# Optimization experiments

Hardware: AMD Instinct MI355X
Metric: run time of the kernel (lower is better)

The kernel has to match this reference:

```python
import jax, jax.numpy as jnp
import numpy as np

MU = 0.9
STEP = 0.1
BETA = 0.999
EPS = 1e-6

N, H, D, M = 256, 16, 64, 64


def elu_feature_map(x):
    # elu(x) + 1, applied to last dim of queries/keys
    return jax.nn.elu(x) + 1.0


def setup_inputs() -> dict:
    key = jax.random.key(0)
    ks = jax.random.split(key, 7)
    return {
        "query": jax.random.normal(ks[0], (N, H, D), dtype=jnp.float32),
        "key": jax.random.normal(ks[1], (N, H, D), dtype=jnp.float32),
        "value": jax.random.normal(ks[2], (N, H, M), dtype=jnp.float32),
        "Si": jax.random.normal(ks[3], (N, H, D, M), dtype=jnp.float32) * 0.1,
        "Zi": jax.random.uniform(ks[4], (N, H, D), dtype=jnp.float32),
        "Pi": jax.random.normal(ks[5], (N, H, D, M), dtype=jnp.float32) * 0.1,
        "Mi": jax.random.uniform(ks[6], (N, H, D, M), dtype=jnp.float32),
        "time_indx": 5,
    }


def reference(query, key, value, Si, Zi, Pi, Mi, time_indx):
    t = time_indx + 1  # Python int -> branch below is static
    Q = elu_feature_map(query)  # (N,H,D)
    K = elu_feature_map(key)    # (N,H,D)

    Zi = Zi + K
    Ui = jnp.einsum('nhd,nhm->nhdm', K, value)  # outer product per (n,h)
    Pi = (MU * Pi - STEP * Ui) * ((1.0 - MU) / (STEP * (1.0 - MU ** t)))
    Mi = BETA * Mi + (1.0 - BETA) * (Ui * Ui)

    rho = 2.0 / (1.0 - BETA) - 1.0
    rhoi = rho - 2.0 * t * BETA ** t / (1.0 - BETA ** t)
    if rhoi > 4.0:
        ri = float(np.sqrt((rhoi - 4.0) * (rhoi - 2.0) * rho
                           / ((rho - 4.0) * (rho - 2.0) * rhoi)))
        Si = Si - Pi * ri / jnp.sqrt(Mi / (1.0 - BETA ** t) + 1e-16)
    else:
        Si = Si - Pi

    Z = 1.0 / (jnp.einsum('nhd,nhd->nh', Q, Zi) + EPS)       # (N,H)
    V = jnp.einsum('nhd,nhdm,nh->nhm', Q, Si, Z)              # (N,H,M)
    return (V, Si, Zi, Pi, Mi)
```

## Files before the change

### kernel.cpp

```cpp
#include <hip/hip_runtime.h>
#include <cmath>

#define D 64
#define M 64

typedef float f4 __attribute__((ext_vector_type(4)));

__global__ __launch_bounds__(256) void raa_kernel(
    const float* __restrict__ q, const float* __restrict__ kk,
    const float* __restrict__ vv, const float* __restrict__ Si,
    const float* __restrict__ Zi, const float* __restrict__ Pi,
    const float* __restrict__ Mi, const int* __restrict__ tind,
    float* __restrict__ oV, float* __restrict__ oSi, float* __restrict__ oZi,
    float* __restrict__ oPi, float* __restrict__ oMi)
{
  const int nh = blockIdx.x;
  const int t  = threadIdx.x;
  const int base = nh * D;
  const int big  = nh * (D * M);

  __shared__ float sQ[D];
  __shared__ float sK[D];
  __shared__ float sVv[M];
  __shared__ float sZ1;
  __shared__ float vred[4][16][4];

  const int ti = tind[0] + 1;
  const double td = (double)ti;
  const double mu_t   = pow(0.9, td);
  const double beta_t = pow(0.999, td);
  const float c1     = (float)(1.0 / (1.0 - mu_t));
  const float inv_bc = (float)(1.0 / (1.0 - beta_t));
  const double rho  = 2.0 / (1.0 - 0.999) - 1.0;
  const double rhoi = rho - 2.0 * td * beta_t / (1.0 - beta_t);
  const bool  use_ri = (rhoi > 4.0);
  const float ri = use_ri
      ? (float)sqrt((rhoi - 4.0) * (rhoi - 2.0) * rho /
                    ((rho - 4.0) * (rho - 2.0) * rhoi))
      : 0.0f;
  const float muf   = 0.9f;
  const float stepf = 0.1f;
  const float betaf = 0.999f;
  const float ombf  = (float)(1.0 - 0.999);

  const int tx = t & 15;
  const int ty = t >> 4;
  const int off0 = big + ty * M + tx * 4;
  f4 pi[4], mi[4], si[4];
#pragma unroll
  for (int j = 0; j < 4; ++j) {
    const int off = off0 + j * (16 * M);
    pi[j] = __builtin_nontemporal_load((const f4*)&Pi[off]);
    mi[j] = __builtin_nontemporal_load((const f4*)&Mi[off]);
    si[j] = __builtin_nontemporal_load((const f4*)&Si[off]);
  }

  if (t < D) {
    const float x = q[base + t];
    const float y = kk[base + t];
    const float Qv = x > 0.f ? x + 1.f : expf(x);
    const float Kv = y > 0.f ? y + 1.f : expf(y);
    const float zn = Zi[base + t] + Kv;
    sQ[t] = Qv;
    sK[t] = Kv;
    sVv[t] = vv[base + t];
    oZi[base + t] = zn;
    float p = Qv * zn;
    p += __shfl_xor(p, 1);
    p += __shfl_xor(p, 2);
    p += __shfl_xor(p, 4);
    p += __shfl_xor(p, 8);
    p += __shfl_xor(p, 16);
    p += __shfl_xor(p, 32);
    if (t == 0) sZ1 = 1.0f / (p + 1e-6f);
  }
  __syncthreads();

  const f4 val4 = *(const f4*)&sVv[tx * 4];
  f4 acc = (f4)(0.f);

#pragma unroll
  for (int j = 0; j < 4; ++j) {
    const int d = ty + 16 * j;
    const int off = off0 + j * (16 * M);
    const float Kd = sK[d];
    const float Qd = sQ[d];

    f4 u  = Kd * val4;
    f4 pn = (muf * pi[j] - stepf * u) * c1;
    f4 mn = betaf * mi[j] + ombf * (u * u);
    __builtin_nontemporal_store(pn, (f4*)&oPi[off]);
    __builtin_nontemporal_store(mn, (f4*)&oMi[off]);

    f4 sn;
    if (use_ri) {
      sn.x = si[j].x - pn.x * ri * rsqrtf(mn.x * inv_bc + 1e-16f);
      sn.y = si[j].y - pn.y * ri * rsqrtf(mn.y * inv_bc + 1e-16f);
      sn.z = si[j].z - pn.z * ri * rsqrtf(mn.z * inv_bc + 1e-16f);
      sn.w = si[j].w - pn.w * ri * rsqrtf(mn.w * inv_bc + 1e-16f);
    } else {
      sn = si[j] - pn;
    }
    __builtin_nontemporal_store(sn, (f4*)&oSi[off]);

    acc += Qd * sn;
  }

  acc.x += __shfl_xor(acc.x, 16); acc.x += __shfl_xor(acc.x, 32);
  acc.y += __shfl_xor(acc.y, 16); acc.y += __shfl_xor(acc.y, 32);
  acc.z += __shfl_xor(acc.z, 16); acc.z += __shfl_xor(acc.z, 32);
  acc.w += __shfl_xor(acc.w, 16); acc.w += __shfl_xor(acc.w, 32);

  const int wave = t >> 6;
  const int lane = t & 63;
  if (lane < 16) {
    vred[wave][lane][0] = acc.x;
    vred[wave][lane][1] = acc.y;
    vred[wave][lane][2] = acc.z;
    vred[wave][lane][3] = acc.w;
  }
  __syncthreads();

  if (t < M) {
    const int mtx = t >> 2, mc = t & 3;
    const float s = vred[0][mtx][mc] + vred[1][mtx][mc] +
                    vred[2][mtx][mc] + vred[3][mtx][mc];
    oV[nh * M + t] = sZ1 * s;
  }
}

extern "C" void kernel_launch(void* const* d_in, const int* in_sizes, int n_in,
                              void* d_out, int out_size, void* d_ws, size_t ws_size,
                              hipStream_t stream) {
  const float* q   = (const float*)d_in[0];
  const float* kk  = (const float*)d_in[1];
  const float* vv  = (const float*)d_in[2];
  const float* Si  = (const float*)d_in[3];
  const float* Zi  = (const float*)d_in[4];
  const float* Pi  = (const float*)d_in[5];
  const float* Mi  = (const float*)d_in[6];
  const int*  tind = (const int*)d_in[7];

  float* out = (float*)d_out;
  float* oV  = out;
  float* oSi = oV  + in_sizes[2];
  float* oZi = oSi + in_sizes[3];
  float* oPi = oZi + in_sizes[4];
  float* oMi = oPi + in_sizes[5];

  const int NH = in_sizes[0] / D;
  raa_kernel<<<NH, 256, 0, stream>>>(q, kk, vv, Si, Zi, Pi, Mi, tind,
                                     oV, oSi, oZi, oPi, oMi);
}
```

Measured before the change: 78.10 us.

## Process four head slices per block with a serial chunk loop

Each block now handles four (n,h) slices: it computes the feature maps, Zi update and normaliser for all four at once, then loops over the chunks to update Pi, Mi and Si and reduce V. The intent is to amortise per-block setup (the pow/sqrt scalar math and the small vector loads) and reduce the block count. In exchange, each block's big-tensor loads are serialised per chunk, and fewer blocks are in flight, which can reduce memory-level parallelism.

```diff
diff --git a/kernel.cpp b/kernel.cpp
--- a/kernel.cpp
+++ b/kernel.cpp
@@ -3,10 +3,11 @@
 
 #define D 64
 #define M 64
+#define CHUNKS 4
 
 typedef float f4 __attribute__((ext_vector_type(4)));
 
-__global__ __launch_bounds__(256) void raa_kernel(
+__global__ __launch_bounds__(256, 4) void raa_kernel(
     const float* __restrict__ q, const float* __restrict__ kk,
     const float* __restrict__ vv, const float* __restrict__ Si,
     const float* __restrict__ Zi, const float* __restrict__ Pi,
@@ -14,16 +15,15 @@
     float* __restrict__ oV, float* __restrict__ oSi, float* __restrict__ oZi,
     float* __restrict__ oPi, float* __restrict__ oMi)
 {
-  const int nh = blockIdx.x;
-  const int t  = threadIdx.x;
-  const int base = nh * D;
-  const int big  = nh * (D * M);
+  const int t   = threadIdx.x;
+  const int nh0 = blockIdx.x * CHUNKS;
 
-  __shared__ float sQ[D];
-  __shared__ float sK[D];
-  __shared__ float sVv[M];
-  __shared__ float sZ1;
-  __shared__ float vred[4][16][4];
+  __shared__ float sQ[CHUNKS][D];
+  __shared__ float sK[CHUNKS][D];
+  __shared__ float sVv[CHUNKS][M];
+  __shared__ float sZn[CHUNKS][D];
+  __shared__ float sZ1[CHUNKS];
+  __shared__ float vred[CHUNKS][4][16][4];
 
   const int ti = tind[0] + 1;
   const double td = (double)ti;
@@ -43,89 +43,102 @@
   const float betaf = 0.999f;
   const float ombf  = (float)(1.0 - 0.999);
 
-  const int tx = t & 15;
-  const int ty = t >> 4;
-  const int off0 = big + ty * M + tx * 4;
-  f4 pi[4], mi[4], si[4];
-#pragma unroll
-  for (int j = 0; j < 4; ++j) {
-    const int off = off0 + j * (16 * M);
-    pi[j] = __builtin_nontemporal_load((const f4*)&Pi[off]);
-    mi[j] = __builtin_nontemporal_load((const f4*)&Mi[off]);
-    si[j] = __builtin_nontemporal_load((const f4*)&Si[off]);
-  }
-
-  if (t < D) {
-    const float x = q[base + t];
-    const float y = kk[base + t];
+  {
+    const int i = nh0 * D + t;
+    const float x = q[i];
+    const float y = kk[i];
     const float Qv = x > 0.f ? x + 1.f : expf(x);
     const float Kv = y > 0.f ? y + 1.f : expf(y);
-    const float zn = Zi[base + t] + Kv;
-    sQ[t] = Qv;
-    sK[t] = Kv;
-    sVv[t] = vv[base + t];
-    oZi[base + t] = zn;
-    float p = Qv * zn;
+    const float zn = Zi[i] + Kv;
+    const int c = t >> 6, l = t & 63;
+    sQ[c][l]  = Qv;
+    sK[c][l]  = Kv;
+    sVv[c][l] = vv[i];
+    sZn[c][l] = zn;
+    oZi[i] = zn;
+  }
+  __syncthreads();
+
+  {
+    const int w = t >> 6, l = t & 63;
+    float p = sQ[w][l] * sZn[w][l];
     p += __shfl_xor(p, 1);
     p += __shfl_xor(p, 2);
     p += __shfl_xor(p, 4);
     p += __shfl_xor(p, 8);
     p += __shfl_xor(p, 16);
     p += __shfl_xor(p, 32);
-    if (t == 0) sZ1 = 1.0f / (p + 1e-6f);
+    if (l == 0) sZ1[w] = 1.0f / (p + 1e-6f);
+  }
+
+  const int tx   = t & 15;
+  const int ty   = t >> 4;
+  const int wave = t >> 6;
+  const int lane = t & 63;
+
+#pragma unroll 1
+  for (int c = 0; c < CHUNKS; ++c) {
+    const int off0 = (nh0 + c) * (D * M) + ty * M + tx * 4;
+
+    f4 pi[4], mi[4], si[4];
+#pragma unroll
+    for (int j = 0; j < 4; ++j) {
+      const int off = off0 + j * (16 * M);
+      pi[j] = __builtin_nontemporal_load((const f4*)&Pi[off]);
+      mi[j] = __builtin_nontemporal_load((const f4*)&Mi[off]);
+      si[j] = __builtin_nontemporal_load((const f4*)&Si[off]);
+    }
+
+    const f4 val4 = *(const f4*)&sVv[c][tx * 4];
+    f4 acc = (f4)(0.f);
+
+#pragma unroll
+    for (int j = 0; j < 4; ++j) {
+      const int d = ty + 16 * j;
+      const int off = off0 + j * (16 * M);
+      const float Kd = sK[c][d];
+      const float Qd = sQ[c][d];
+
+      f4 u  = Kd * val4;
+      f4 pn = (muf * pi[j] - stepf * u) * c1;
+      f4 mn = betaf * mi[j] + ombf * (u * u);
+      __builtin_nontemporal_store(pn, (f4*)&oPi[off]);
+      __builtin_nontemporal_store(mn, (f4*)&oMi[off]);
+
+      f4 sn;
+      if (use_ri) {
+        sn.x = si[j].x - pn.x * ri * rsqrtf(mn.x * inv_bc + 1e-16f);
+        sn.y = si[j].y - pn.y * ri * rsqrtf(mn.y * inv_bc + 1e-16f);
+        sn.z = si[j].z - pn.z * ri * rsqrtf(mn.z * inv_bc + 1e-16f);
+        sn.w = si[j].w - pn.w * ri * rsqrtf(mn.w * inv_bc + 1e-16f);
+      } else {
+        sn = si[j] - pn;
+      }
+      __builtin_nontemporal_store(sn, (f4*)&oSi[off]);
+
+      acc += Qd * sn;
+    }
+
+    acc.x += __shfl_xor(acc.x, 16); acc.x += __shfl_xor(acc.x, 32);
+    acc.y += __shfl_xor(acc.y, 16); acc.y += __shfl_xor(acc.y, 32);
+    acc.z += __shfl_xor(acc.z, 16); acc.z += __shfl_xor(acc.z, 32);
+    acc.w += __shfl_xor(acc.w, 16); acc.w += __shfl_xor(acc.w, 32);
+
+    if (lane < 16) {
+      vred[c][wave][lane][0] = acc.x;
+      vred[c][wave][lane][1] = acc.y;
+      vred[c][wave][lane][2] = acc.z;
+      vred[c][wave][lane][3] = acc.w;
+    }
   }
   __syncthreads();
 
-  const f4 val4 = *(const f4*)&sVv[tx * 4];
-  f4 acc = (f4)(0.f);
-
-#pragma unroll
-  for (int j = 0; j < 4; ++j) {
-    const int d = ty + 16 * j;
-    const int off = off0 + j * (16 * M);
-    const float Kd = sK[d];
-    const float Qd = sQ[d];
-
-    f4 u  = Kd * val4;
-    f4 pn = (muf * pi[j] - stepf * u) * c1;
-    f4 mn = betaf * mi[j] + ombf * (u * u);
-    __builtin_nontemporal_store(pn, (f4*)&oPi[off]);
-    __builtin_nontemporal_store(mn, (f4*)&oMi[off]);
-
-    f4 sn;
-    if (use_ri) {
-      sn.x = si[j].x - pn.x * ri * rsqrtf(mn.x * inv_bc + 1e-16f);
-      sn.y = si[j].y - pn.y * ri * rsqrtf(mn.y * inv_bc + 1e-16f);
-      sn.z = si[j].z - pn.z * ri * rsqrtf(mn.z * inv_bc + 1e-16f);
-      sn.w = si[j].w - pn.w * ri * rsqrtf(mn.w * inv_bc + 1e-16f);
-    } else {
-      sn = si[j] - pn;
-    }
-    __builtin_nontemporal_store(sn, (f4*)&oSi[off]);
-
-    acc += Qd * sn;
-  }
-
-  acc.x += __shfl_xor(acc.x, 16); acc.x += __shfl_xor(acc.x, 32);
-  acc.y += __shfl_xor(acc.y, 16); acc.y += __shfl_xor(acc.y, 32);
-  acc.z += __shfl_xor(acc.z, 16); acc.z += __shfl_xor(acc.z, 32);
-  acc.w += __shfl_xor(acc.w, 16); acc.w += __shfl_xor(acc.w, 32);
-
-  const int wave = t >> 6;
-  const int lane = t & 63;
-  if (lane < 16) {
-    vred[wave][lane][0] = acc.x;
-    vred[wave][lane][1] = acc.y;
-    vred[wave][lane][2] = acc.z;
-    vred[wave][lane][3] = acc.w;
-  }
-  __syncthreads();
-
-  if (t < M) {
-    const int mtx = t >> 2, mc = t & 3;
-    const float s = vred[0][mtx][mc] + vred[1][mtx][mc] +
-                    vred[2][mtx][mc] + vred[3][mtx][mc];
-    oV[nh * M + t] = sZ1 * s;
+  {
+    const int c = t >> 6, m = t & 63;
+    const int mtx = m >> 2, mc = m & 3;
+    const float s = vred[c][0][mtx][mc] + vred[c][1][mtx][mc] +
+                    vred[c][2][mtx][mc] + vred[c][3][mtx][mc];
+    oV[nh0 * M + t] = sZ1[c] * s;
   }
 }
 
@@ -149,6 +162,6 @@
   float* oMi = oPi + in_sizes[5];
 
   const int NH = in_sizes[0] / D;
-  raa_kernel<<<NH, 256, 0, stream>>>(q, kk, vv, Si, Zi, Pi, Mi, tind,
-                                     oV, oSi, oZi, oPi, oMi);
+  raa_kernel<<<NH / CHUNKS, 256, 0, stream>>>(q, kk, vv, Si, Zi, Pi, Mi, tind,
+                                              oV, oSi, oZi, oPi, oMi);
 }
```

New measurement: 80.54 us. +3.1%, slower.
